# Optimization experiments

Measured on AMD Instinct MI355X. Metric: run time of the kernel, lower is better.

The kernel has to match this reference:

```python
import jax, jax.numpy as jnp
import numpy as np

STEP = 0.175
K = 128  # static bin cap; randn data at step 0.175 needs ~70 bins, so clipping is a no-op


def _bin_idx(x, step):
    # pd.cut(data, bins=arange(floor(min), ceil(max)+step, step)): interval (b[i], b[i+1]]
    # -> idx = ceil((x - lower)/step) - 1. Labels (bin midpoints) are bijective with idx,
    # so all downstream Counter/entropy math can run on integer bin indices directly.
    lower = jnp.floor(jnp.min(x))
    return jnp.clip(jnp.ceil((x - lower) / step) - 1, 0, K - 1).astype(jnp.int32)


def _row_entropy(codes):
    # plug-in Shannon entropy (natural log, like scipy.stats.entropy) per row:
    # H = log n - mean_j log(count of codes[j]); counts via sort + searchsorted runs
    s = jnp.sort(codes, axis=1)
    left = jax.vmap(lambda r: jnp.searchsorted(r, r, side='left'))(s)
    right = jax.vmap(lambda r: jnp.searchsorted(r, r, side='right'))(s)
    cnt = (right - left).astype(jnp.float32)
    return jnp.log(jnp.float32(codes.shape[1])) - jnp.mean(jnp.log(cnt), axis=1)


def _soft_ce(logits, target):
    # F.cross_entropy with soft targets, reduction='mean' (mean over batch)
    return jnp.mean(-jnp.sum(target * jax.nn.log_softmax(logits, -1), axis=-1))


def _kl_mean(logits, target):
    # F.kl_div(log_softmax(logits), target, reduction='mean') -> mean over ALL elements
    logp = jax.nn.log_softmax(logits, -1)
    return jnp.mean(target * (jnp.log(target) - logp))


def _H_out(logits, target):
    return _soft_ce(logits, target) - _kl_mean(logits, target)


def setup_inputs() -> dict:
    key = jax.random.key(0)
    ks = jax.random.split(key, 8)
    B, D = 4096, 1024
    return {
        'data': jax.random.normal(ks[0], (B, 3 * D), jnp.float32),
        'data1': jax.random.normal(ks[1], (B, D), jnp.float32),
        'data2': jax.random.normal(ks[2], (B, D), jnp.float32),
        'data3': jax.random.normal(ks[3], (B, D), jnp.float32),
        'output1': jax.random.normal(ks[4], (B, D), jnp.float32),
        'output2': jax.random.normal(ks[5], (B, D), jnp.float32),
        'output3': jax.random.normal(ks[6], (B, D), jnp.float32),
        'output': jax.random.normal(ks[7], (B, 3 * D), jnp.float32),
    }


def reference(data, data1, data2, data3, output1, output2, output3, output):
    cat = lambda xs: jnp.concatenate(xs, axis=1)
    mse = 0.5 * jnp.mean((data - output) ** 2)

    # discretized histogram/entropy path runs on .detach()'d numpy in torch -> stop_gradient
    i1 = _bin_idx(jax.lax.stop_gradient(data1), STEP)
    i2 = _bin_idx(jax.lax.stop_gradient(data2), STEP)
    i3 = _bin_idx(jax.lax.stop_gradient(data3), STEP)

    H_d1 = jnp.mean(_row_entropy(i1))
    H_d2 = jnp.mean(_row_entropy(i2))
    H_d3 = jnp.mean(_row_entropy(i3))

    p1 = jax.nn.softmax(data1, -1)
    p2 = jax.nn.softmax(data2, -1)
    p3 = jax.nn.softmax(data3, -1)
    H_o1 = _H_out(output1, p1)
    H_o2 = _H_out(output2, p2)
    H_o3 = _H_out(output3, p3)

    H_1 = H_d1 - H_o1
    H_2 = H_d2 - H_o2
    H_3 = H_d3 - H_o3

    # ave_joint_entropy over padded label matrices == joint entropy of (idx_x, idx_y) pairs
    # (equal column counts -> pad_matrices is a no-op; labels<->indices are bijective)
    H_in_13 = jnp.mean(_row_entropy(i1 * K + i3))
    H_in_23 = jnp.mean(_row_entropy(i2 * K + i3))
    H_in_12 = jnp.mean(_row_entropy(i1 * K + i2))

    H_o13 = _H_out(cat([output1, output3]), jax.nn.softmax(cat([data1, data3]), -1))
    H_o23 = _H_out(cat([output2, output3]), jax.nn.softmax(cat([data2, data3]), -1))
    H_o12 = _H_out(cat([output1, output2]), jax.nn.softmax(cat([data1, data2]), -1))

    H_MI13 = (H_o1 + H_o3 - H_o13) - (H_d1 + H_d3 - H_in_13)
    H_MI23 = (H_o2 + H_o3 - H_o23) - (H_d2 + H_d3 - H_in_23)
    H_MI12 = (H_o1 + H_o2 - H_o12) - (H_d1 + H_d2 - H_in_12)

    # per-row conditional MI I(x1; x2 | x3) = H(1,3)+H(2,3)-H(3)-H(1,2,3), SUMMED over rows
    c123 = (i1 * K + i2) * K + i3
    cmi_rows = (_row_entropy(i1 * K + i3) + _row_entropy(i2 * K + i3)
                - _row_entropy(i3) - _row_entropy(c123))
    data_mu = jnp.sum(cmi_rows)

    H_o123 = _H_out(cat([output1, output2, output3]),
                    jax.nn.softmax(cat([data1, data2, data3]), -1))
    label_cmi = H_o23 - H_o3 + H_o13 - H_o123
    CMI = label_cmi - data_mu

    return 0.9 * mse + 0.1 * (H_1 ** 2 + H_2 ** 2 + H_3 ** 2
                              + H_MI13 ** 2 + H_MI23 ** 2 + H_MI12 ** 2 + CMI ** 2)
```

## Files before the change

### kernel.cpp

```cpp
#include <hip/hip_runtime.h>
#include <stdint.h>

#define ROWS 4096
#define NCOL 1024
#define NT 256
#define NBANK 64
#define BSTRIDE 32

#define NB 72
#define ROWB 76
#define PAIRW (NB * (ROWB / 4))
#define TRIW 1536
#define T23_BASE PAIRW
#define T31_BASE (2 * PAIRW)
#define TRI_BASE (3 * PAIRW)
#define TABW (3 * PAIRW + TRIW)


__device__ __forceinline__ uint32_t f2ord(float f) {
  uint32_t b = __float_as_uint(f);
  return (b & 0x80000000u) ? ~b : (b | 0x80000000u);
}
__device__ __forceinline__ float ord2f(uint32_t u) {
  uint32_t b = (u & 0x80000000u) ? (u & 0x7FFFFFFFu) : ~u;
  return __uint_as_float(b);
}

__device__ __forceinline__ float wave_sum(float x) {
  float t;
  t = __int_as_float(__builtin_amdgcn_update_dpp(0, __float_as_int(x), 0x111, 0xf, 0xf, false)); x += t;
  t = __int_as_float(__builtin_amdgcn_update_dpp(0, __float_as_int(x), 0x112, 0xf, 0xf, false)); x += t;
  t = __int_as_float(__builtin_amdgcn_update_dpp(0, __float_as_int(x), 0x114, 0xf, 0xf, false)); x += t;
  t = __int_as_float(__builtin_amdgcn_update_dpp(0, __float_as_int(x), 0x118, 0xf, 0xf, false)); x += t;
  t = __int_as_float(__builtin_amdgcn_update_dpp(0, __float_as_int(x), 0x142, 0xa, 0xf, false)); x += t;
  t = __int_as_float(__builtin_amdgcn_update_dpp(0, __float_as_int(x), 0x143, 0xc, 0xf, false)); x += t;
  return x;
}

__global__ __launch_bounds__(256) void k_pre(
    const float4* __restrict__ d1, const float4* __restrict__ d2,
    const float4* __restrict__ d3, uint32_t* __restrict__ minb) {
  __shared__ float sred[4];
  const int t = threadIdx.x;
  const float4* p = (blockIdx.y == 0) ? d1 : (blockIdx.y == 1) ? d2 : d3;
  const int n4 = ROWS * NCOL / 4;
  float lm = 1e30f;
  for (int i = blockIdx.x * 256 + t; i < n4; i += gridDim.x * 256) {
    float4 v = p[i];
    lm = fminf(lm, fminf(fminf(v.x, v.y), fminf(v.z, v.w)));
  }
  for (int o = 32; o > 0; o >>= 1) lm = fminf(lm, __shfl_down(lm, o, 64));
  if ((t & 63) == 0) sred[t >> 6] = lm;
  __syncthreads();
  if (t == 0) {
    lm = fminf(fminf(sred[0], sred[1]), fminf(sred[2], sred[3]));
    atomicMax(&minb[blockIdx.y], ~f2ord(lm));
  }
}

__device__ __noinline__ void hslow(uint32_t* __restrict__ tri, uint32_t key,
                                   uint32_t slot) {
  for (;;) {
    ++slot;
    if (slot == TRIW) slot = 0;
    uint32_t cur = tri[slot];
    if ((cur >> 11) == key) { atomicAdd((unsigned int*)&tri[slot], 1u); return; }
    if (cur == 0u) {
      uint32_t old = atomicCAS((unsigned int*)&tri[slot], 0u, (key << 11) | 1u);
      if (old == 0u) return;
      if ((old >> 11) == key) { atomicAdd((unsigned int*)&tri[slot], 1u); return; }
    }
  }
}

__device__ __forceinline__ uint32_t bini(float x, float low) {
  return (uint32_t)min(max((int)ceilf((x - low) * (1.0f / 0.175f)) - 1, 0),
                       NB - 1);
}

__global__ __launch_bounds__(NT, 7) void k_row(
    const float* __restrict__ d1, const float* __restrict__ d2,
    const float* __restrict__ d3, const float* __restrict__ o1,
    const float* __restrict__ o2, const float* __restrict__ o3,
    const float4* __restrict__ data, const float4* __restrict__ outp,
    const uint32_t* __restrict__ minb, float* __restrict__ acc) {
  __shared__ __align__(16) uint32_t tab[TABW];
  __shared__ float sA[4][12];
  __shared__ float sB[4][8];
  const int r = blockIdx.x, t = threadIdx.x;
  float* bank = acc + (r & (NBANK - 1)) * BSTRIDE;

#pragma unroll
  for (int i = t; i < TABW / 4; i += NT) ((uint4*)tab)[i] = make_uint4(0, 0, 0, 0);

  const float low1 = floorf(ord2f(~minb[0]));
  const float low2 = floorf(ord2f(~minb[1]));
  const float low3 = floorf(ord2f(~minb[2]));

  const size_t off = (size_t)r * NCOL;
  const float4 x1 = ((const float4*)(d1 + off))[t];
  const float4 x2 = ((const float4*)(d2 + off))[t];
  const float4 x3 = ((const float4*)(d3 + off))[t];
  const float xd[3][4] = {{x1.x, x1.y, x1.z, x1.w},
                          {x2.x, x2.y, x2.z, x2.w},
                          {x3.x, x3.y, x3.z, x3.w}};
  uint32_t b1[4], b2[4], b3[4];
#pragma unroll
  for (int u = 0; u < 4; ++u) {
    b1[u] = bini(xd[0][u], low1);
    b2[u] = bini(xd[1][u], low2);
    b3[u] = bini(xd[2][u], low3);
  }
  __syncthreads();

#pragma unroll
  for (int u = 0; u < 4; ++u) {
    const uint32_t i12 = b1[u] * ROWB + b2[u];
    const uint32_t i23 = b2[u] * ROWB + b3[u];
    const uint32_t i31 = b3[u] * ROWB + b1[u];
    atomicAdd((unsigned int*)&tab[i12 >> 2], 1u << ((i12 & 3u) * 8u));
    atomicAdd((unsigned int*)&tab[T23_BASE + (i23 >> 2)], 1u << ((i23 & 3u) * 8u));
    atomicAdd((unsigned int*)&tab[T31_BASE + (i31 >> 2)], 1u << ((i31 & 3u) * 8u));
  }

  const float4 y1 = ((const float4*)(o1 + off))[t];
  const float4 y2 = ((const float4*)(o2 + off))[t];
  const float4 y3 = ((const float4*)(o3 + off))[t];

  uint32_t key[4], slot[4], old[4];
#pragma unroll
  for (int u = 0; u < 4; ++u) {
    key[u] = (b1[u] << 14) | (b2[u] << 7) | b3[u];
    uint32_t h = (key[u] * 2654435761u) >> 21;
    slot[u] = (h * 3u) >> 2;
    old[u] = atomicCAS((unsigned int*)&tab[TRI_BASE + slot[u]], 0u,
                       (key[u] << 11) | 1u);
  }
#pragma unroll
  for (int u = 0; u < 4; ++u) {
    if (old[u] != 0u) {
      if ((old[u] >> 11) == key[u])
        atomicAdd((unsigned int*)&tab[TRI_BASE + slot[u]], 1u);
      else
        hslow(tab + TRI_BASE, key[u], slot[u]);
    }
  }

  float ms = 0.f;
  {
    const float4* pa = data + (size_t)r * 768;
    const float4* pb = outp + (size_t)r * 768;
#pragma unroll
    for (int u = 0; u < 3; ++u) {
      float4 a0 = pa[t + u * NT], bq = pb[t + u * NT];
      float dx = a0.x - bq.x, dy = a0.y - bq.y, dz = a0.z - bq.z, dw = a0.w - bq.w;
      ms += dx * dx + dy * dy + dz * dz + dw * dw;
    }
  }

  const float xo[3][4] = {{y1.x, y1.y, y1.z, y1.w},
                          {y2.x, y2.y, y2.z, y2.w},
                          {y3.x, y3.y, y3.z, y3.w}};
  float v[12];
#pragma unroll
  for (int k = 0; k < 3; ++k) {
    float E = 0.f, F = 0.f, G = 0.f, LE = 0.f;
#pragma unroll
    for (int u = 0; u < 4; ++u) {
      float w = __expf(xd[k][u]);
      E += w;
      F += w * xd[k][u];
      G += w * xo[k][u];
      LE += __expf(xo[k][u]);
    }
    v[k * 4 + 0] = E; v[k * 4 + 1] = F; v[k * 4 + 2] = G; v[k * 4 + 3] = LE;
  }
#pragma unroll
  for (int j = 0; j < 12; ++j) v[j] = wave_sum(v[j]);
  if ((t & 63) == 63)
#pragma unroll
    for (int j = 0; j < 12; ++j) sA[t >> 6][j] = v[j];
  __syncthreads();

  float rS1 = 0.f, rS2 = 0.f, rS3 = 0.f, rS12 = 0.f, rS13 = 0.f, rS23 = 0.f,
        rS123 = 0.f;
  if (t < 3 * NB) {
    const int tbl = t / NB, row = t - tbl * NB;
    const uint32_t base = (uint32_t)tbl * PAIRW + (uint32_t)row * (ROWB / 4);
    uint32_t rs4 = 0;
    float pl = 0.f;
#pragma unroll
    for (int w = 0; w < 18; ++w) {
      uint32_t vv = tab[base + w];
      rs4 += vv;
      if (vv & 0xFEFEFEFEu) {
#pragma unroll
        for (int bq = 0; bq < 4; ++bq) {
          uint32_t c = (vv >> (8 * bq)) & 255u;
          if (c > 1u) { float fc = (float)c; pl += fc * __logf(fc); }
        }
      }
    }
    uint32_t s2 = (rs4 & 0x00FF00FFu) + ((rs4 >> 8) & 0x00FF00FFu);
    uint32_t rowsum = (s2 + (s2 >> 16)) & 0xFFFFu;
    float fr = (rowsum > 1u) ? (float)rowsum * __logf((float)rowsum) : 0.f;
    if (tbl == 0) { rS12 = pl; rS1 = fr; }
    else if (tbl == 1) { rS23 = pl; rS2 = fr; }
    else { rS13 = pl; rS3 = fr; }
  }
  for (int i = t; i < TRIW / 4; i += NT) {
    uint4 e = ((const uint4*)(tab + TRI_BASE))[i];
    uint32_t c0 = e.x & 0x7FFu, c1 = e.y & 0x7FFu, c2 = e.z & 0x7FFu,
             c3 = e.w & 0x7FFu;
    if (c0 > 1u) { float fc = (float)c0; rS123 += fc * __logf(fc); }
    if (c1 > 1u) { float fc = (float)c1; rS123 += fc * __logf(fc); }
    if (c2 > 1u) { float fc = (float)c2; rS123 += fc * __logf(fc); }
    if (c3 > 1u) { float fc = (float)c3; rS123 += fc * __logf(fc); }
  }

  float p[8];
  p[0] = rS1; p[1] = rS2; p[2] = rS3; p[3] = rS12;
  p[4] = rS13; p[5] = rS23; p[6] = rS123; p[7] = ms;
#pragma unroll
  for (int j = 0; j < 8; ++j) p[j] = wave_sum(p[j]);
  if ((t & 63) == 63)
#pragma unroll
    for (int j = 0; j < 8; ++j) sB[t >> 6][j] = p[j];
  __syncthreads();

  if (t < 16) {
    if (t < 7) {
      const int masks[7] = {1, 2, 4, 5, 6, 3, 7};
      const int m = masks[t];
      float Z = 0.f, Fs = 0.f, Gs = 0.f, LZ = 0.f;
#pragma unroll
      for (int k = 0; k < 3; ++k)
        if (m & (1 << k)) {
#pragma unroll
          for (int w = 0; w < 4; ++w) {
            Z += sA[w][k * 4 + 0];
            Fs += sA[w][k * 4 + 1];
            Gs += sA[w][k * 4 + 2];
            LZ += sA[w][k * 4 + 3];
          }
        }
      const float rZ = 1.0f / Z;
      const float T = Fs * rZ - __logf(Z);
      const float A = -(Gs * rZ) + __logf(LZ);
      atomicAdd(&bank[8 + t], A);
      atomicAdd(&bank[15 + t], T);
    } else if (t < 15) {
      const int j = t - 8;
      atomicAdd(&bank[1 + j], sB[0][j] + sB[1][j] + sB[2][j] + sB[3][j]);
    } else {
      atomicAdd(&bank[0], sB[0][7] + sB[1][7] + sB[2][7] + sB[3][7]);
    }
  }
}

__global__ void k_final(const float* __restrict__ acc, float* __restrict__ out) {
  const int t = threadIdx.x;
  double q[22];
#pragma unroll
  for (int i = 0; i < 22; ++i) q[i] = (double)acc[t * BSTRIDE + i];
#pragma unroll
  for (int o = 32; o > 0; o >>= 1)
#pragma unroll
    for (int i = 0; i < 22; ++i) q[i] += __shfl_down(q[i], o, 64);
  if (t != 0) return;

  const double logn = log(1024.0);
  const double Rn = 4096.0 * 1024.0;
  double Hd1 = logn - q[1] / Rn, Hd2 = logn - q[2] / Rn, Hd3 = logn - q[3] / Rn;
  double Hin12 = logn - q[4] / Rn, Hin13 = logn - q[5] / Rn, Hin23 = logn - q[6] / Rn;
  double data_mu = (q[3] + q[7] - q[5] - q[6]) / 1024.0;

  auto hout = [](double A, double T, double D) {
    return (1.0 - 1.0 / D) * A / 4096.0 - T / (4096.0 * D);
  };
  double Ho1 = hout(q[8], q[15], 1024.0);
  double Ho2 = hout(q[9], q[16], 1024.0);
  double Ho3 = hout(q[10], q[17], 1024.0);
  double Ho13 = hout(q[11], q[18], 2048.0);
  double Ho23 = hout(q[12], q[19], 2048.0);
  double Ho12 = hout(q[13], q[20], 2048.0);
  double Ho123 = hout(q[14], q[21], 3072.0);

  double H1 = Hd1 - Ho1, H2 = Hd2 - Ho2, H3 = Hd3 - Ho3;
  double MI13 = (Ho1 + Ho3 - Ho13) - (Hd1 + Hd3 - Hin13);
  double MI23 = (Ho2 + Ho3 - Ho23) - (Hd2 + Hd3 - Hin23);
  double MI12 = (Ho1 + Ho2 - Ho12) - (Hd1 + Hd2 - Hin12);
  double label_cmi = Ho23 - Ho3 + Ho13 - Ho123;
  double CMI = label_cmi - data_mu;
  double mse = 0.5 * q[0] / (4096.0 * 3072.0);
  out[0] = (float)(0.9 * mse +
                   0.1 * (H1 * H1 + H2 * H2 + H3 * H3 + MI13 * MI13 +
                          MI23 * MI23 + MI12 * MI12 + CMI * CMI));
}

extern "C" void kernel_launch(void* const* d_in, const int* in_sizes, int n_in,
                              void* d_out, int out_size, void* d_ws, size_t ws_size,
                              hipStream_t stream) {
  const float* data  = (const float*)d_in[0];
  const float* data1 = (const float*)d_in[1];
  const float* data2 = (const float*)d_in[2];
  const float* data3 = (const float*)d_in[3];
  const float* out1  = (const float*)d_in[4];
  const float* out2  = (const float*)d_in[5];
  const float* out3  = (const float*)d_in[6];
  const float* outp  = (const float*)d_in[7];
  float* acc = (float*)d_ws;
  uint32_t* minb = (uint32_t*)((float*)d_ws + NBANK * BSTRIDE);

  hipMemsetAsync(acc, 0, NBANK * BSTRIDE * sizeof(float) + 3 * sizeof(uint32_t),
                 stream);
  k_pre<<<dim3(256, 3), 256, 0, stream>>>((const float4*)data1,
                                          (const float4*)data2,
                                          (const float4*)data3, minb);
  k_row<<<ROWS, NT, 0, stream>>>(data1, data2, data3, out1, out2, out3,
                                 (const float4*)data, (const float4*)outp,
                                 minb, acc);
  k_final<<<1, 64, 0, stream>>>(acc, (float*)d_out);
}
```

Measured before the change: 240.1 us.

## Drop memset and final kernel, fuse finalize via last-block counter

Removes the hipMemsetAsync and the separate k_final launch. k_pre now zeroes the accumulators and writes per-block minima, and the last k_row block, found through an atomic ticket counter, does the final reduction. Shared tables are shrunk (ROWB 72, hash table 1148 slots) and occupancy is raised to 8 blocks per SM. Each k_row block now reduces 384 partial minima itself. This cuts launch and memset overhead but adds a serial tail reduction and per-block redundant min work.

```diff
diff --git a/kernel.cpp b/kernel.cpp
--- a/kernel.cpp
+++ b/kernel.cpp
@@ -5,26 +5,19 @@
 #define NCOL 1024
 #define NT 256
 #define NBANK 64
-#define BSTRIDE 32
+#define BSTRIDE 24
 
 #define NB 72
-#define ROWB 76
+#define ROWB 72
 #define PAIRW (NB * (ROWB / 4))
-#define TRIW 1536
+#define TRIW 1148
 #define T23_BASE PAIRW
 #define T31_BASE (2 * PAIRW)
 #define TRI_BASE (3 * PAIRW)
 #define TABW (3 * PAIRW + TRIW)
 
-
-__device__ __forceinline__ uint32_t f2ord(float f) {
-  uint32_t b = __float_as_uint(f);
-  return (b & 0x80000000u) ? ~b : (b | 0x80000000u);
-}
-__device__ __forceinline__ float ord2f(uint32_t u) {
-  uint32_t b = (u & 0x80000000u) ? (u & 0x7FFFFFFFu) : ~u;
-  return __uint_as_float(b);
-}
+#define CNT_OFF 1536
+#define MINP_OFF 1540
 
 __device__ __forceinline__ float wave_sum(float x) {
   float t;
@@ -37,15 +30,19 @@
   return x;
 }
 
-__global__ __launch_bounds__(256) void k_pre(
+__global__ __launch_bounds__(512) void k_pre(
     const float4* __restrict__ d1, const float4* __restrict__ d2,
-    const float4* __restrict__ d3, uint32_t* __restrict__ minb) {
-  __shared__ float sred[4];
+    const float4* __restrict__ d3, float* __restrict__ ws) {
+  __shared__ float sred[8];
   const int t = threadIdx.x;
+  if (blockIdx.y == 0 && blockIdx.x < 4) {
+    const int idx = blockIdx.x * 512 + t;
+    if (idx < MINP_OFF) ((uint32_t*)ws)[idx] = 0u;
+  }
   const float4* p = (blockIdx.y == 0) ? d1 : (blockIdx.y == 1) ? d2 : d3;
   const int n4 = ROWS * NCOL / 4;
   float lm = 1e30f;
-  for (int i = blockIdx.x * 256 + t; i < n4; i += gridDim.x * 256) {
+  for (int i = blockIdx.x * 512 + t; i < n4; i += gridDim.x * 512) {
     float4 v = p[i];
     lm = fminf(lm, fminf(fminf(v.x, v.y), fminf(v.z, v.w)));
   }
@@ -53,8 +50,9 @@
   if ((t & 63) == 0) sred[t >> 6] = lm;
   __syncthreads();
   if (t == 0) {
-    lm = fminf(fminf(sred[0], sred[1]), fminf(sred[2], sred[3]));
-    atomicMax(&minb[blockIdx.y], ~f2ord(lm));
+#pragma unroll
+    for (int w = 1; w < 8; ++w) lm = fminf(lm, sred[w]);
+    ws[MINP_OFF + blockIdx.y * 128 + blockIdx.x] = lm;
   }
 }
 
@@ -78,29 +76,49 @@
                        NB - 1);
 }
 
-__global__ __launch_bounds__(NT, 7) void k_row(
+__global__ __launch_bounds__(NT, 8) void k_row(
     const float* __restrict__ d1, const float* __restrict__ d2,
     const float* __restrict__ d3, const float* __restrict__ o1,
     const float* __restrict__ o2, const float* __restrict__ o3,
     const float4* __restrict__ data, const float4* __restrict__ outp,
-    const uint32_t* __restrict__ minb, float* __restrict__ acc) {
+    float* __restrict__ ws, float* __restrict__ out) {
   __shared__ __align__(16) uint32_t tab[TABW];
   __shared__ float sA[4][12];
   __shared__ float sB[4][8];
+  __shared__ uint32_t sLast;
   const int r = blockIdx.x, t = threadIdx.x;
+  float* acc = ws;
+  uint32_t* cnt = (uint32_t*)(ws + CNT_OFF);
+  const float* minpart = ws + MINP_OFF;
   float* bank = acc + (r & (NBANK - 1)) * BSTRIDE;
 
-#pragma unroll
-  for (int i = t; i < TABW / 4; i += NT) ((uint4*)tab)[i] = make_uint4(0, 0, 0, 0);
-
-  const float low1 = floorf(ord2f(~minb[0]));
-  const float low2 = floorf(ord2f(~minb[1]));
-  const float low3 = floorf(ord2f(~minb[2]));
-
+  float m1 = 1e30f, m2 = 1e30f, m3 = 1e30f;
+  if (t < 128) {
+    m1 = minpart[t]; m2 = minpart[128 + t]; m3 = minpart[256 + t];
+  }
   const size_t off = (size_t)r * NCOL;
   const float4 x1 = ((const float4*)(d1 + off))[t];
   const float4 x2 = ((const float4*)(d2 + off))[t];
   const float4 x3 = ((const float4*)(d3 + off))[t];
+
+#pragma unroll
+  for (int i = t; i < TABW / 4; i += NT) ((uint4*)tab)[i] = make_uint4(0, 0, 0, 0);
+
+#pragma unroll
+  for (int o = 32; o > 0; o >>= 1) {
+    m1 = fminf(m1, __shfl_down(m1, o, 64));
+    m2 = fminf(m2, __shfl_down(m2, o, 64));
+    m3 = fminf(m3, __shfl_down(m3, o, 64));
+  }
+  if ((t & 63) == 0) {
+    sB[t >> 6][0] = m1; sB[t >> 6][1] = m2; sB[t >> 6][2] = m3;
+  }
+  __syncthreads();
+
+  const float low1 = floorf(fminf(fminf(sB[0][0], sB[1][0]), fminf(sB[2][0], sB[3][0])));
+  const float low2 = floorf(fminf(fminf(sB[0][1], sB[1][1]), fminf(sB[2][1], sB[3][1])));
+  const float low3 = floorf(fminf(fminf(sB[0][2], sB[1][2]), fminf(sB[2][2], sB[3][2])));
+
   const float xd[3][4] = {{x1.x, x1.y, x1.z, x1.w},
                           {x2.x, x2.y, x2.z, x2.w},
                           {x3.x, x3.y, x3.z, x3.w}};
@@ -111,7 +129,6 @@
     b2[u] = bini(xd[1][u], low2);
     b3[u] = bini(xd[2][u], low3);
   }
-  __syncthreads();
 
 #pragma unroll
   for (int u = 0; u < 4; ++u) {
@@ -132,7 +149,7 @@
   for (int u = 0; u < 4; ++u) {
     key[u] = (b1[u] << 14) | (b2[u] << 7) | b3[u];
     uint32_t h = (key[u] * 2654435761u) >> 21;
-    slot[u] = (h * 3u) >> 2;
+    slot[u] = (h * (uint32_t)TRIW) >> 11;
     old[u] = atomicCAS((unsigned int*)&tab[TRI_BASE + slot[u]], 0u,
                        (key[u] << 11) | 1u);
   }
@@ -230,8 +247,7 @@
 
   if (t < 16) {
     if (t < 7) {
-      const int masks[7] = {1, 2, 4, 5, 6, 3, 7};
-      const int m = masks[t];
+      const int m = (int)((0x7365421u >> (4 * t)) & 0xFu);
       float Z = 0.f, Fs = 0.f, Gs = 0.f, LZ = 0.f;
 #pragma unroll
       for (int k = 0; k < 3; ++k)
@@ -256,46 +272,54 @@
       atomicAdd(&bank[0], sB[0][7] + sB[1][7] + sB[2][7] + sB[3][7]);
     }
   }
-}
-
-__global__ void k_final(const float* __restrict__ acc, float* __restrict__ out) {
-  const int t = threadIdx.x;
-  double q[22];
-#pragma unroll
-  for (int i = 0; i < 22; ++i) q[i] = (double)acc[t * BSTRIDE + i];
-#pragma unroll
-  for (int o = 32; o > 0; o >>= 1)
-#pragma unroll
-    for (int i = 0; i < 22; ++i) q[i] += __shfl_down(q[i], o, 64);
-  if (t != 0) return;
-
+
+  __syncthreads();
+  if (t == 0)
+    sLast = (__hip_atomic_fetch_add(cnt, 1u, __ATOMIC_ACQ_REL,
+                                    __HIP_MEMORY_SCOPE_AGENT) == ROWS - 1u)
+                ? 1u : 0u;
+  __syncthreads();
+  if (sLast == 0u || t >= 64) return;
+
+  auto red = [&](int i) -> double {
+    double s = (double)__hip_atomic_load(&acc[t * BSTRIDE + i], __ATOMIC_RELAXED,
+                                         __HIP_MEMORY_SCOPE_AGENT);
+#pragma unroll
+    for (int o = 32; o > 0; o >>= 1) s += __shfl_down(s, o, 64);
+    return s;
+  };
   const double logn = log(1024.0);
   const double Rn = 4096.0 * 1024.0;
-  double Hd1 = logn - q[1] / Rn, Hd2 = logn - q[2] / Rn, Hd3 = logn - q[3] / Rn;
-  double Hin12 = logn - q[4] / Rn, Hin13 = logn - q[5] / Rn, Hin23 = logn - q[6] / Rn;
-  double data_mu = (q[3] + q[7] - q[5] - q[6]) / 1024.0;
+  double S1 = red(1), S2 = red(2), S3 = red(3), S12 = red(4), S13 = red(5),
+         S23 = red(6), S123 = red(7);
+  double Hd1 = logn - S1 / Rn, Hd2 = logn - S2 / Rn, Hd3 = logn - S3 / Rn;
+  double Hin12 = logn - S12 / Rn, Hin13 = logn - S13 / Rn, Hin23 = logn - S23 / Rn;
+  double data_mu = (S3 + S123 - S13 - S23) / 1024.0;
 
   auto hout = [](double A, double T, double D) {
     return (1.0 - 1.0 / D) * A / 4096.0 - T / (4096.0 * D);
   };
-  double Ho1 = hout(q[8], q[15], 1024.0);
-  double Ho2 = hout(q[9], q[16], 1024.0);
-  double Ho3 = hout(q[10], q[17], 1024.0);
-  double Ho13 = hout(q[11], q[18], 2048.0);
-  double Ho23 = hout(q[12], q[19], 2048.0);
-  double Ho12 = hout(q[13], q[20], 2048.0);
-  double Ho123 = hout(q[14], q[21], 3072.0);
-
-  double H1 = Hd1 - Ho1, H2 = Hd2 - Ho2, H3 = Hd3 - Ho3;
-  double MI13 = (Ho1 + Ho3 - Ho13) - (Hd1 + Hd3 - Hin13);
-  double MI23 = (Ho2 + Ho3 - Ho23) - (Hd2 + Hd3 - Hin23);
-  double MI12 = (Ho1 + Ho2 - Ho12) - (Hd1 + Hd2 - Hin12);
-  double label_cmi = Ho23 - Ho3 + Ho13 - Ho123;
-  double CMI = label_cmi - data_mu;
-  double mse = 0.5 * q[0] / (4096.0 * 3072.0);
-  out[0] = (float)(0.9 * mse +
-                   0.1 * (H1 * H1 + H2 * H2 + H3 * H3 + MI13 * MI13 +
-                          MI23 * MI23 + MI12 * MI12 + CMI * CMI));
+  double Ho1 = hout(red(8), red(15), 1024.0);
+  double Ho2 = hout(red(9), red(16), 1024.0);
+  double Ho3 = hout(red(10), red(17), 1024.0);
+  double Ho13 = hout(red(11), red(18), 2048.0);
+  double Ho23 = hout(red(12), red(19), 2048.0);
+  double Ho12 = hout(red(13), red(20), 2048.0);
+  double Ho123 = hout(red(14), red(21), 3072.0);
+  double mseq = red(0);
+
+  if (t == 0) {
+    double H1 = Hd1 - Ho1, H2 = Hd2 - Ho2, H3 = Hd3 - Ho3;
+    double MI13 = (Ho1 + Ho3 - Ho13) - (Hd1 + Hd3 - Hin13);
+    double MI23 = (Ho2 + Ho3 - Ho23) - (Hd2 + Hd3 - Hin23);
+    double MI12 = (Ho1 + Ho2 - Ho12) - (Hd1 + Hd2 - Hin12);
+    double label_cmi = Ho23 - Ho3 + Ho13 - Ho123;
+    double CMI = label_cmi - data_mu;
+    double mse = 0.5 * mseq / (4096.0 * 3072.0);
+    out[0] = (float)(0.9 * mse +
+                     0.1 * (H1 * H1 + H2 * H2 + H3 * H3 + MI13 * MI13 +
+                            MI23 * MI23 + MI12 * MI12 + CMI * CMI));
+  }
 }
 
 extern "C" void kernel_launch(void* const* d_in, const int* in_sizes, int n_in,
@@ -309,16 +333,12 @@
   const float* out2  = (const float*)d_in[5];
   const float* out3  = (const float*)d_in[6];
   const float* outp  = (const float*)d_in[7];
-  float* acc = (float*)d_ws;
-  uint32_t* minb = (uint32_t*)((float*)d_ws + NBANK * BSTRIDE);
-
-  hipMemsetAsync(acc, 0, NBANK * BSTRIDE * sizeof(float) + 3 * sizeof(uint32_t),
-                 stream);
-  k_pre<<<dim3(256, 3), 256, 0, stream>>>((const float4*)data1,
+  float* ws = (float*)d_ws;
+
+  k_pre<<<dim3(128, 3), 512, 0, stream>>>((const float4*)data1,
                                           (const float4*)data2,
-                                          (const float4*)data3, minb);
+                                          (const float4*)data3, ws);
   k_row<<<ROWS, NT, 0, stream>>>(data1, data2, data3, out1, out2, out3,
                                  (const float4*)data, (const float4*)outp,
-                                 minb, acc);
-  k_final<<<1, 64, 0, stream>>>(acc, (float*)d_out);
-}
+                                 ws, (float*)d_out);
+}
```

Result: slower. 450.5 us (+87.6%).
